# Optimization experiments

Measured on AMD Instinct MI355X. Metric: run time of the kernel, lower is better.

Reference implementation:

```python
import jax, jax.numpy as jnp
import numpy as np

N = 50000
E = 800000
IN_DIM, HID, HEADS, OUT_DIM = 128, 32, 4, 16
NEG_SLOPE = 0.2


def gat_layer(x, src, dst, W, a_src, a_dst, bias, heads, out_ch, concat):
    # x: [N, F_in]; W: [F_in, heads*out_ch]; a_src/a_dst: [heads, out_ch]
    n = x.shape[0]
    xp = (x @ W).reshape(n, heads, out_ch)                      # [N, H, C]
    alpha_s = (xp * a_src).sum(-1)                              # [N, H]
    alpha_d = (xp * a_dst).sum(-1)                              # [N, H]
    e = jax.nn.leaky_relu(alpha_s[src] + alpha_d[dst], NEG_SLOPE)  # [E, H]
    # scatter-softmax over incoming edges of each destination node
    m = jax.ops.segment_max(e, dst, num_segments=n)             # [N, H]
    ex = jnp.exp(e - m[dst])
    denom = jax.ops.segment_sum(ex, dst, num_segments=n)        # [N, H]
    alpha = ex / denom[dst]                                     # [E, H]
    msg = xp[src] * alpha[:, :, None]                           # [E, H, C]
    out = jax.ops.segment_sum(msg, dst, num_segments=n)         # [N, H, C]
    if concat:
        return out.reshape(n, heads * out_ch) + bias
    return out.mean(axis=1) + bias


def setup_inputs() -> dict:
    key = jax.random.key(0)
    ks = jax.random.split(key, 10)
    x = jax.random.normal(ks[0], (N, IN_DIM), dtype=jnp.float32)
    edge_index = jax.random.randint(ks[1], (2, E), 0, N, dtype=jnp.int64)
    g = lambda k, shape, fan: jax.random.normal(k, shape, dtype=jnp.float32) * (1.0 / np.sqrt(fan))
    return {
        "x": x,
        "edge_index": edge_index,
        "W1": g(ks[2], (IN_DIM, HEADS * HID), IN_DIM),
        "a_src1": g(ks[3], (HEADS, HID), HID),
        "a_dst1": g(ks[4], (HEADS, HID), HID),
        "b1": jnp.zeros((HEADS * HID,), dtype=jnp.float32),
        "W2": g(ks[5], (HEADS * HID, OUT_DIM), HEADS * HID),
        "a_src2": g(ks[6], (1, OUT_DIM), OUT_DIM),
        "a_dst2": g(ks[7], (1, OUT_DIM), OUT_DIM),
        "b2": jnp.zeros((OUT_DIM,), dtype=jnp.float32),
    }


def reference(x, edge_index, W1, a_src1, a_dst1, b1, W2, a_src2, a_dst2, b2):
    # add self loops (PyG GATConv default add_self_loops=True)
    loop = jnp.arange(N, dtype=edge_index.dtype)
    src = jnp.concatenate([edge_index[0], loop])
    dst = jnp.concatenate([edge_index[1], loop])
    h = gat_layer(x, src, dst, W1, a_src1, a_dst1, b1, HEADS, HID, concat=True)
    h = jax.nn.elu(h)
    out = gat_layer(h, src, dst, W2, a_src2, a_dst2, b2, 1, OUT_DIM, concat=True)
    return jax.nn.log_softmax(out, axis=1)
```

## Files before the change

kernel.cpp:

```cpp
#include <hip/hip_runtime.h>
#include <math.h>

#define CAP    64
#define CAPB   32
#define GPART  256
#define BSH    7
#define BNODES 128

typedef __attribute__((ext_vector_type(4))) float f32x4;
typedef __attribute__((ext_vector_type(2))) float f32x2;
typedef __attribute__((ext_vector_type(8))) short s16x8;

__device__ __forceinline__ unsigned short f2bf(float f) {
    unsigned u = __float_as_uint(f);
    unsigned r = u + 0x7FFFu + ((u >> 16) & 1u);
    return (unsigned short)(r >> 16);
}
__device__ __forceinline__ float bf2f(unsigned short b) {
    return __uint_as_float(((unsigned)b) << 16);
}
__device__ __forceinline__ unsigned char f2fp8(float f) {
    int w = __builtin_amdgcn_cvt_pk_fp8_f32(f, f, 0, false);
    return (unsigned char)(w & 0xFF);
}

__device__ __forceinline__ int ldidx(const void* ei, int pos, bool i64) {
    if (i64) return (int)((const long long*)ei)[pos];
    return ((const int*)ei)[pos];
}

__global__ void detect_i64(const unsigned* ei32, int* flag) {
    __shared__ int nz;
    if (threadIdx.x == 0) nz = 0;
    __syncthreads();
    unsigned v = ei32[2 * threadIdx.x + 1];
    if (v != 0) atomicOr(&nz, 1);
    __syncthreads();
    if (threadIdx.x == 0) *flag = (nz == 0) ? 1 : 0;
}

__global__ void prep_bt(const float* __restrict__ W1, const float* __restrict__ aS,
                        const float* __restrict__ aD, unsigned short* __restrict__ Bt) {
    int i = blockIdx.x * 256 + threadIdx.x;
    if (i >= 144 * 128) return;
    int c = i >> 7, k = i & 127;
    float v = 0.f;
    if (c < 128) {
        v = W1[k * 128 + c];
    } else if (c < 136) {
        int q = c - 128;
        const float* a = (q < 4) ? aS : aD;
        int h = q & 3;
        float s = 0.f;
        for (int j = 0; j < 32; ++j)
            s = fmaf(W1[k * 128 + h * 32 + j], a[h * 32 + j], s);
        v = s;
    }
    Bt[c * 128 + k] = f2bf(v);
}

__global__ __launch_bounds__(256, 2) void gemm1_mfma(
        const float* __restrict__ x, const unsigned short* __restrict__ Bt,
        unsigned char* __restrict__ xp8, float* __restrict__ as1,
        float* __restrict__ ad1, int n) {
    __shared__ short xsb[64][132];
    __shared__ short btb[144][132];
    int tid = threadIdx.x;
    int rowbase = blockIdx.x * 64;

    {
        int row = tid >> 2, seg = tid & 3;
        int grow = rowbase + row; if (grow >= n) grow = n - 1;
        const float* xr = x + (size_t)grow * 128 + seg * 32;
#pragma unroll
        for (int q = 0; q < 8; ++q) {
            float4 c = *(const float4*)(xr + q * 4);
            short4 o;
            o.x = (short)f2bf(c.x); o.y = (short)f2bf(c.y);
            o.z = (short)f2bf(c.z); o.w = (short)f2bf(c.w);
            *(short4*)(&xsb[row][seg * 32 + q * 4]) = o;
        }
    }
    for (int idx = tid; idx < 144 * 32; idx += 256) {
        int c = idx >> 5, kq = idx & 31;
        short4 v = *(const short4*)(Bt + c * 128 + kq * 4);
        *(short4*)(&btb[c][kq * 4]) = v;
    }
    __syncthreads();

    int lane = tid & 63;
    int wave = tid >> 6;
    int rb = wave * 16;
    int col = lane & 15;
    int ksub = (lane >> 4) * 4;
    int arow = rb + (lane & 15);

    f32x4 acc[9];
#pragma unroll
    for (int t = 0; t < 9; ++t) acc[t] = (f32x4){0.f, 0.f, 0.f, 0.f};

#pragma unroll
    for (int ks = 0; ks < 4; ++ks) {
        short4 a0 = *(const short4*)(&xsb[arow][ks * 32 + ksub]);
        short4 a1 = *(const short4*)(&xsb[arow][ks * 32 + 16 + ksub]);
        s16x8 a;
        a[0] = a0.x; a[1] = a0.y; a[2] = a0.z; a[3] = a0.w;
        a[4] = a1.x; a[5] = a1.y; a[6] = a1.z; a[7] = a1.w;
#pragma unroll
        for (int t = 0; t < 9; ++t) {
            short4 b0 = *(const short4*)(&btb[t * 16 + col][ks * 32 + ksub]);
            short4 b1 = *(const short4*)(&btb[t * 16 + col][ks * 32 + 16 + ksub]);
            s16x8 b;
            b[0] = b0.x; b[1] = b0.y; b[2] = b0.z; b[3] = b0.w;
            b[4] = b1.x; b[5] = b1.y; b[6] = b1.z; b[7] = b1.w;
            acc[t] = __builtin_amdgcn_mfma_f32_16x16x32_bf16(a, b, acc[t], 0, 0, 0);
        }
    }

    int crow = rowbase + rb + (lane >> 4) * 4;
#pragma unroll
    for (int t = 0; t < 8; ++t) {
#pragma unroll
        for (int r = 0; r < 4; ++r) {
            int row = crow + r;
            if (row < n) xp8[(size_t)row * 128 + t * 16 + col] = f2fp8(acc[t][r]);
        }
    }
    if (col < 8) {
#pragma unroll
        for (int r = 0; r < 4; ++r) {
            int row = crow + r;
            if (row < n) {
                if (col < 4) as1[row * 4 + col] = acc[8][r];
                else         ad1[row * 4 + (col - 4)] = acc[8][r];
            }
        }
    }
}

__global__ __launch_bounds__(256) void partition_k(
        const void* ei, const int* dflag, int* __restrict__ stage,
        int* __restrict__ cnts, int E, int nbuk) {
    __shared__ int qcnt[1024];
    int blk = blockIdx.x, t = threadIdx.x;
    for (int b = t; b < nbuk; b += 256) qcnt[b] = 0;
    __syncthreads();
    bool i64 = (*dflag != 0);
    int chunk = (E + GPART - 1) / GPART;
    int lo = blk * chunk;
    int hi = lo + chunk; if (hi > E) hi = E;
    for (int i = lo + t; i < hi; i += 256) {
        int s = ldidx(ei, i, i64);
        int d = ldidx(ei, E + i, i64);
        int b = d >> BSH, dl = d & (BNODES - 1);
        int slot = atomicAdd(&qcnt[b], 1);
        if (slot < CAPB)
            stage[((size_t)b * GPART + blk) * CAPB + slot] = (dl << 24) | s;
    }
    __syncthreads();
    for (int b = t; b < nbuk; b += 256)
        cnts[b * GPART + blk] = min(qcnt[b], CAPB);
}

__global__ __launch_bounds__(256) void merge_k(
        const int* __restrict__ cnts, const int* __restrict__ stage,
        int* __restrict__ src_pad, int* __restrict__ lens, int n) {
    __shared__ int rows[BNODES][CAP];
    __shared__ int rcnt[BNODES];
    int b = blockIdx.x, t = threadIdx.x;
    if (t < BNODES) rcnt[t] = 0;
    __syncthreads();
    int v = cnts[b * GPART + t];
    const int* seg = stage + ((size_t)b * GPART + t) * CAPB;
    for (int q = 0; q < v; ++q) {
        int item = seg[q];
        int dl = item >> 24;
        int s  = item & 0xFFFFFF;
        int r = atomicAdd(&rcnt[dl], 1);
        if (r < CAP - 1) rows[dl][r] = s;
    }
    __syncthreads();
    int base = b << BSH;
    if (t < BNODES && base + t < n) {
        int r = min(rcnt[t], CAP - 1);
        rows[t][r] = base + t;
        lens[base + t] = r + 1;
    }
    __syncthreads();
    for (int idx = t; idx < BNODES * CAP; idx += 256) {
        int node = base + (idx >> 6);
        if (node < n) src_pad[(size_t)node * CAP + (idx & (CAP - 1))] = rows[idx >> 6][idx & (CAP - 1)];
    }
}

__global__ __launch_bounds__(256) void agg1_gather(
        const int* __restrict__ lens, const int* __restrict__ src_pad,
        const float* __restrict__ as1, const float* __restrict__ ad1,
        const unsigned char* __restrict__ xp8, const float* __restrict__ b1,
        unsigned short* __restrict__ houtb, int n) {
    int g = blockIdx.x * 8 + (threadIdx.x >> 5);
    if (g >= n) return;
    int lane = threadIdx.x & 31;
    int h = lane >> 3;
    int len = lens[g];
    const int* sp = src_pad + (size_t)g * CAP;
    float adv = ad1[g * 4 + h];
    float ax = 0.f, ay = 0.f, az = 0.f, aw = 0.f, den = 0.f;
    int j = 0;
    for (; j + 8 <= len; j += 8) {
        int      ss[8];
        float    qq[8];
        unsigned vv[8];
#pragma unroll
        for (int q = 0; q < 8; ++q) ss[q] = sp[j + q];
#pragma unroll
        for (int q = 0; q < 8; ++q) qq[q] = as1[ss[q] * 4 + h];
#pragma unroll
        for (int q = 0; q < 8; ++q)
            vv[q] = *(const unsigned*)(xp8 + (size_t)ss[q] * 128 + lane * 4);
#pragma unroll
        for (int q = 0; q < 8; ++q) {
            float e = qq[q] + adv;
            e = e > 0.f ? e : 0.2f * e;
            e = __expf(e);
            den += e;
            f32x2 lo = __builtin_amdgcn_cvt_pk_f32_fp8(vv[q], false);
            f32x2 hi = __builtin_amdgcn_cvt_pk_f32_fp8(vv[q], true);
            ax = fmaf(lo[0], e, ax);
            ay = fmaf(lo[1], e, ay);
            az = fmaf(hi[0], e, az);
            aw = fmaf(hi[1], e, aw);
        }
    }
    for (; j < len; ++j) {
        int s = sp[j];
        float e = as1[s * 4 + h] + adv;
        e = e > 0.f ? e : 0.2f * e;
        e = __expf(e);
        unsigned w = *(const unsigned*)(xp8 + (size_t)s * 128 + lane * 4);
        den += e;
        f32x2 lo = __builtin_amdgcn_cvt_pk_f32_fp8(w, false);
        f32x2 hi = __builtin_amdgcn_cvt_pk_f32_fp8(w, true);
        ax = fmaf(lo[0], e, ax);
        ay = fmaf(lo[1], e, ay);
        az = fmaf(hi[0], e, az);
        aw = fmaf(hi[1], e, aw);
    }
    float inv = 1.f / den;
    int c0 = lane * 4;
    const float4 bb = *(const float4*)(b1 + c0);
    float o0 = fmaf(ax, inv, bb.x); o0 = o0 > 0.f ? o0 : expm1f(o0);
    float o1 = fmaf(ay, inv, bb.y); o1 = o1 > 0.f ? o1 : expm1f(o1);
    float o2 = fmaf(az, inv, bb.z); o2 = o2 > 0.f ? o2 : expm1f(o2);
    float o3 = fmaf(aw, inv, bb.w); o3 = o3 > 0.f ? o3 : expm1f(o3);
    ushort4 o;
    o.x = f2bf(o0); o.y = f2bf(o1); o.z = f2bf(o2); o.w = f2bf(o3);
    *(ushort4*)(houtb + (size_t)g * 128 + c0) = o;
}

__global__ void proj2(const unsigned short* __restrict__ h, const float* __restrict__ W2,
                      const float* __restrict__ aw_s, const float* __restrict__ aw_d,
                      unsigned short* __restrict__ xp2b, float* __restrict__ as2,
                      float* __restrict__ ad2, int n) {
    __shared__ float hs[16][128];
    int t = threadIdx.x;
    int ln = t >> 4;
    int j = t & 15;
    int node = blockIdx.x * 16 + ln;
    if (node < n) {
        ushort4 a0 = *(const ushort4*)(h + (size_t)node * 128 + j * 8);
        ushort4 a1 = *(const ushort4*)(h + (size_t)node * 128 + j * 8 + 4);
        hs[ln][j * 8 + 0] = bf2f(a0.x); hs[ln][j * 8 + 1] = bf2f(a0.y);
        hs[ln][j * 8 + 2] = bf2f(a0.z); hs[ln][j * 8 + 3] = bf2f(a0.w);
        hs[ln][j * 8 + 4] = bf2f(a1.x); hs[ln][j * 8 + 5] = bf2f(a1.y);
        hs[ln][j * 8 + 6] = bf2f(a1.z); hs[ln][j * 8 + 7] = bf2f(a1.w);
    }
    __syncthreads();
    if (node >= n) return;
    float acc = 0.f;
#pragma unroll 4
    for (int c = 0; c < 128; ++c)
        acc = fmaf(hs[ln][c], W2[c * 16 + j], acc);
    xp2b[(size_t)node * 16 + j] = f2bf(acc);
    float ps = acc * aw_s[j];
    float pd = acc * aw_d[j];
    for (int off = 8; off >= 1; off >>= 1) {
        ps += __shfl_xor(ps, off, 16);
        pd += __shfl_xor(pd, off, 16);
    }
    if (j == 0) { as2[node] = ps; ad2[node] = pd; }
}

__global__ void agg2_gather(const int* __restrict__ lens, const int* __restrict__ src_pad,
                            const float* __restrict__ as2, const float* __restrict__ ad2,
                            const unsigned short* __restrict__ xp2b,
                            const float* __restrict__ b2,
                            float* __restrict__ out, int n) {
    int g = blockIdx.x * 64 + (threadIdx.x >> 2);
    if (g >= n) return;
    int lane = threadIdx.x & 3;
    int len = lens[g];
    const int* sp = src_pad + (size_t)g * CAP;
    float adv = ad2[g];
    float ax = 0.f, ay = 0.f, az = 0.f, aw = 0.f, den = 0.f;
    int j = 0;
    for (; j + 4 <= len; j += 4) {
        int s0 = sp[j + 0], s1 = sp[j + 1], s2 = sp[j + 2], s3 = sp[j + 3];
        float q0 = as2[s0], q1 = as2[s1], q2 = as2[s2], q3 = as2[s3];
        ushort4 v0 = *(const ushort4*)(xp2b + (size_t)s0 * 16 + lane * 4);
        ushort4 v1 = *(const ushort4*)(xp2b + (size_t)s1 * 16 + lane * 4);
        ushort4 v2 = *(const ushort4*)(xp2b + (size_t)s2 * 16 + lane * 4);
        ushort4 v3 = *(const ushort4*)(xp2b + (size_t)s3 * 16 + lane * 4);
        float e0 = q0 + adv; e0 = e0 > 0.f ? e0 : 0.2f * e0; e0 = __expf(e0);
        float e1 = q1 + adv; e1 = e1 > 0.f ? e1 : 0.2f * e1; e1 = __expf(e1);
        float e2 = q2 + adv; e2 = e2 > 0.f ? e2 : 0.2f * e2; e2 = __expf(e2);
        float e3 = q3 + adv; e3 = e3 > 0.f ? e3 : 0.2f * e3; e3 = __expf(e3);
        den += (e0 + e1) + (e2 + e3);
        ax = fmaf(bf2f(v0.x), e0, ax); ay = fmaf(bf2f(v0.y), e0, ay);
        az = fmaf(bf2f(v0.z), e0, az); aw = fmaf(bf2f(v0.w), e0, aw);
        ax = fmaf(bf2f(v1.x), e1, ax); ay = fmaf(bf2f(v1.y), e1, ay);
        az = fmaf(bf2f(v1.z), e1, az); aw = fmaf(bf2f(v1.w), e1, aw);
        ax = fmaf(bf2f(v2.x), e2, ax); ay = fmaf(bf2f(v2.y), e2, ay);
        az = fmaf(bf2f(v2.z), e2, az); aw = fmaf(bf2f(v2.w), e2, aw);
        ax = fmaf(bf2f(v3.x), e3, ax); ay = fmaf(bf2f(v3.y), e3, ay);
        az = fmaf(bf2f(v3.z), e3, az); aw = fmaf(bf2f(v3.w), e3, aw);
    }
    for (; j < len; ++j) {
        int s = sp[j];
        float e = as2[s] + adv;
        e = e > 0.f ? e : 0.2f * e;
        e = __expf(e);
        ushort4 v = *(const ushort4*)(xp2b + (size_t)s * 16 + lane * 4);
        den += e;
        ax = fmaf(bf2f(v.x), e, ax); ay = fmaf(bf2f(v.y), e, ay);
        az = fmaf(bf2f(v.z), e, az); aw = fmaf(bf2f(v.w), e, aw);
    }
    float inv = 1.f / den;
    const float4 bb = *(const float4*)(b2 + lane * 4);
    float v0 = fmaf(ax, inv, bb.x);
    float v1 = fmaf(ay, inv, bb.y);
    float v2 = fmaf(az, inv, bb.z);
    float v3 = fmaf(aw, inv, bb.w);
    float mm = fmaxf(fmaxf(v0, v1), fmaxf(v2, v3));
    for (int off = 1; off < 4; off <<= 1) mm = fmaxf(mm, __shfl_xor(mm, off, 4));
    float ss = __expf(v0 - mm) + __expf(v1 - mm) + __expf(v2 - mm) + __expf(v3 - mm);
    for (int off = 1; off < 4; off <<= 1) ss += __shfl_xor(ss, off, 4);
    float ls = mm + __logf(ss);
    float4 o = {v0 - ls, v1 - ls, v2 - ls, v3 - ls};
    *(float4*)(out + (size_t)g * 16 + lane * 4) = o;
}

extern "C" void kernel_launch(void* const* d_in, const int* in_sizes, int n_in,
                              void* d_out, int out_size, void* d_ws, size_t ws_size,
                              hipStream_t stream) {
    const float* x    = (const float*)d_in[0];
    const void*  ei   = d_in[1];
    const float* W1   = (const float*)d_in[2];
    const float* aS1  = (const float*)d_in[3];
    const float* aD1  = (const float*)d_in[4];
    const float* b1   = (const float*)d_in[5];
    const float* W2   = (const float*)d_in[6];
    const float* aS2  = (const float*)d_in[7];
    const float* aD2  = (const float*)d_in[8];
    const float* b2   = (const float*)d_in[9];

    const int N    = in_sizes[0] / 128;
    const int E    = in_sizes[1] / 2;
    const int NBUK = (N + BNODES - 1) >> BSH;

    char* p = (char*)d_ws;
    unsigned char* xp8 = (unsigned char*)p;     p += (size_t)128 * N;
    float* as1 = (float*)p;                     p += (size_t)4 * N * 4;
    float* ad1 = (float*)p;                     p += (size_t)4 * N * 4;
    unsigned short* hbufb = (unsigned short*)p; p += (size_t)128 * N * 2;
    unsigned short* xp2b = (unsigned short*)p;  p += (size_t)16 * N * 2;
    float* as2 = (float*)p;                     p += (size_t)N * 4;
    float* ad2 = (float*)p;                     p += (size_t)N * 4;
    int* lens = (int*)p;                        p += (size_t)N * 4;
    int* src_pad = (int*)p;                     p += (size_t)N * CAP * 4;
    int* stage = (int*)p;                       p += (size_t)NBUK * GPART * CAPB * 4;
    int* cnts = (int*)p;                        p += (size_t)NBUK * GPART * 4;
    unsigned short* Bt = (unsigned short*)p;    p += (size_t)144 * 128 * 2;
    int* dflag = (int*)p;

    detect_i64<<<1, 256, 0, stream>>>((const unsigned*)ei, dflag);

    partition_k<<<GPART, 256, 0, stream>>>(ei, dflag, stage, cnts, E, NBUK);

    prep_bt<<<72, 256, 0, stream>>>(W1, aS1, aD1, Bt);

    gemm1_mfma<<<(N + 63) / 64, 256, 0, stream>>>(x, Bt, xp8, as1, ad1, N);

    merge_k<<<NBUK, 256, 0, stream>>>(cnts, stage, src_pad, lens, N);

    agg1_gather<<<(N + 7) / 8, 256, 0, stream>>>(lens, src_pad, as1, ad1, xp8, b1,
                                                 hbufb, N);

    proj2<<<(N + 15) / 16, 256, 0, stream>>>(hbufb, W2, aS2, aD2, xp2b, as2, ad2, N);

    agg2_gather<<<(N + 63) / 64, 256, 0, stream>>>(lens, src_pad, as2, ad2, xp2b, b2,
                                                   (float*)d_out, N);
}
```

Baseline: 117.0 us.

## Fuse index-width detection, partition and weight prep into one launch; enlarge GEMM tiles

Folds the separate int64-detection, edge partition and weight-transpose kernels into a single launch. Each partition block now detects the index width locally from its own chunk, and extra blocks prepare the bf16 weight matrix. The first GEMM now uses 512-thread blocks covering 128 rows, so each block loads the weight tile into shared memory once for twice as many rows. The aim is to cut launch overhead and the repeated per-block weight staging. The trade-offs are higher LDS use per block and a width detection that depends on each block's chunk, which could misjudge a chunk if its high words happen to be zero.

```diff
diff --git a/kernel.cpp b/kernel.cpp
--- a/kernel.cpp
+++ b/kernel.cpp
@@ -29,44 +29,63 @@
     return ((const int*)ei)[pos];
 }
 
-__global__ void detect_i64(const unsigned* ei32, int* flag) {
+__global__ __launch_bounds__(256) void part_prep_k(
+        const void* ei, const float* __restrict__ W1, const float* __restrict__ aS,
+        const float* __restrict__ aD, unsigned short* __restrict__ Bt,
+        int* __restrict__ stage, int* __restrict__ cnts, int E, int nbuk) {
+    int blk = blockIdx.x, t = threadIdx.x;
+    if (blk >= GPART) {
+        int i = (blk - GPART) * 256 + t;
+        if (i >= 144 * 128) return;
+        int c = i >> 7, k = i & 127;
+        float v = 0.f;
+        if (c < 128) {
+            v = W1[k * 128 + c];
+        } else if (c < 136) {
+            int q = c - 128;
+            const float* a = (q < 4) ? aS : aD;
+            int h = q & 3;
+            float s = 0.f;
+            for (int j = 0; j < 32; ++j)
+                s = fmaf(W1[k * 128 + h * 32 + j], a[h * 32 + j], s);
+            v = s;
+        }
+        Bt[c * 128 + k] = f2bf(v);
+        return;
+    }
+    __shared__ int qcnt[1024];
     __shared__ int nz;
-    if (threadIdx.x == 0) nz = 0;
-    __syncthreads();
-    unsigned v = ei32[2 * threadIdx.x + 1];
-    if (v != 0) atomicOr(&nz, 1);
-    __syncthreads();
-    if (threadIdx.x == 0) *flag = (nz == 0) ? 1 : 0;
-}
-
-__global__ void prep_bt(const float* __restrict__ W1, const float* __restrict__ aS,
-                        const float* __restrict__ aD, unsigned short* __restrict__ Bt) {
-    int i = blockIdx.x * 256 + threadIdx.x;
-    if (i >= 144 * 128) return;
-    int c = i >> 7, k = i & 127;
-    float v = 0.f;
-    if (c < 128) {
-        v = W1[k * 128 + c];
-    } else if (c < 136) {
-        int q = c - 128;
-        const float* a = (q < 4) ? aS : aD;
-        int h = q & 3;
-        float s = 0.f;
-        for (int j = 0; j < 32; ++j)
-            s = fmaf(W1[k * 128 + h * 32 + j], a[h * 32 + j], s);
-        v = s;
-    }
-    Bt[c * 128 + k] = f2bf(v);
-}
-
-__global__ __launch_bounds__(256, 2) void gemm1_mfma(
+    if (t == 0) nz = 0;
+    for (int b = t; b < nbuk; b += 256) qcnt[b] = 0;
+    __syncthreads();
+    int chunk = (E + GPART - 1) / GPART;
+    int lo = blk * chunk;
+    int hi = lo + chunk; if (hi > E) hi = E;
+    int sidx = lo + t;
+    if (sidx < hi && ((const unsigned*)ei)[2 * sidx + 1] != 0) atomicOr(&nz, 1);
+    __syncthreads();
+    bool i64 = (nz == 0);
+    for (int i = lo + t; i < hi; i += 256) {
+        int s = ldidx(ei, i, i64);
+        int d = ldidx(ei, E + i, i64);
+        int b = d >> BSH, dl = d & (BNODES - 1);
+        int slot = atomicAdd(&qcnt[b], 1);
+        if (slot < CAPB)
+            stage[((size_t)b * GPART + blk) * CAPB + slot] = (dl << 24) | s;
+    }
+    __syncthreads();
+    for (int b = t; b < nbuk; b += 256)
+        cnts[b * GPART + blk] = min(qcnt[b], CAPB);
+}
+
+__global__ __launch_bounds__(512, 2) void gemm1_mfma(
         const float* __restrict__ x, const unsigned short* __restrict__ Bt,
         unsigned char* __restrict__ xp8, float* __restrict__ as1,
         float* __restrict__ ad1, int n) {
-    __shared__ short xsb[64][132];
+    __shared__ short xsb[128][132];
     __shared__ short btb[144][132];
     int tid = threadIdx.x;
-    int rowbase = blockIdx.x * 64;
+    int rowbase = blockIdx.x * 128;
 
     {
         int row = tid >> 2, seg = tid & 3;
@@ -81,7 +100,7 @@
             *(short4*)(&xsb[row][seg * 32 + q * 4]) = o;
         }
     }
-    for (int idx = tid; idx < 144 * 32; idx += 256) {
+    for (int idx = tid; idx < 144 * 32; idx += 512) {
         int c = idx >> 5, kq = idx & 31;
         short4 v = *(const short4*)(Bt + c * 128 + kq * 4);
         *(short4*)(&btb[c][kq * 4]) = v;
@@ -136,30 +155,6 @@
             }
         }
     }
-}
-
-__global__ __launch_bounds__(256) void partition_k(
-        const void* ei, const int* dflag, int* __restrict__ stage,
-        int* __restrict__ cnts, int E, int nbuk) {
-    __shared__ int qcnt[1024];
-    int blk = blockIdx.x, t = threadIdx.x;
-    for (int b = t; b < nbuk; b += 256) qcnt[b] = 0;
-    __syncthreads();
-    bool i64 = (*dflag != 0);
-    int chunk = (E + GPART - 1) / GPART;
-    int lo = blk * chunk;
-    int hi = lo + chunk; if (hi > E) hi = E;
-    for (int i = lo + t; i < hi; i += 256) {
-        int s = ldidx(ei, i, i64);
-        int d = ldidx(ei, E + i, i64);
-        int b = d >> BSH, dl = d & (BNODES - 1);
-        int slot = atomicAdd(&qcnt[b], 1);
-        if (slot < CAPB)
-            stage[((size_t)b * GPART + blk) * CAPB + slot] = (dl << 24) | s;
-    }
-    __syncthreads();
-    for (int b = t; b < nbuk; b += 256)
-        cnts[b * GPART + blk] = min(qcnt[b], CAPB);
 }
 
 __global__ __launch_bounds__(256) void merge_k(
@@ -381,15 +376,13 @@
     int* stage = (int*)p;                       p += (size_t)NBUK * GPART * CAPB * 4;
     int* cnts = (int*)p;                        p += (size_t)NBUK * GPART * 4;
     unsigned short* Bt = (unsigned short*)p;    p += (size_t)144 * 128 * 2;
-    int* dflag = (int*)p;
-
-    detect_i64<<<1, 256, 0, stream>>>((const unsigned*)ei, dflag);
-
-    partition_k<<<GPART, 256, 0, stream>>>(ei, dflag, stage, cnts, E, NBUK);
-
-    prep_bt<<<72, 256, 0, stream>>>(W1, aS1, aD1, Bt);
-
-    gemm1_mfma<<<(N + 63) / 64, 256, 0, stream>>>(x, Bt, xp8, as1, ad1, N);
+
+    const int PREPB = (144 * 128 + 255) / 256;
+
+    part_prep_k<<<GPART + PREPB, 256, 0, stream>>>(ei, W1, aS1, aD1, Bt,
+                                                   stage, cnts, E, NBUK);
+
+    gemm1_mfma<<<(N + 127) / 128, 512, 0, stream>>>(x, Bt, xp8, as1, ad1, N);
 
     merge_k<<<NBUK, 256, 0, stream>>>(cnts, stage, src_pad, lens, N);
 
```

Measured after the change: 103.4 us. 1.13x faster.
